# Optimization experiments

Measured on AMD Instinct MI355X. Metric: run time of the kernel, lower is better.

## Reference

```python
import jax, jax.numpy as jnp
import numpy as np

LEAK = 0.01   # torch LeakyReLU default negative_slope
EPS = 1e-5    # torch BatchNorm2d default eps


def setup_inputs() -> dict:
    key = jax.random.key(0)
    ks = jax.random.split(key, 7)
    x = jax.random.normal(ks[0], (1, 64, 512, 512), jnp.float32)
    W = jax.random.normal(ks[1], (128, 64, 3, 3), jnp.float32) * 0.05
    gamma = jax.random.uniform(ks[2], (128,), jnp.float32, 0.5, 1.5)
    beta = jax.random.normal(ks[3], (128,), jnp.float32) * 0.1
    mean = jax.random.normal(ks[4], (128,), jnp.float32) * 0.1
    var = jax.random.uniform(ks[5], (128,), jnp.float32, 0.5, 1.5)
    # random.choices(rate=[0,1,1,...,1]) -> Bernoulli(0.9) mask over (1,C,H*W)
    mask = jax.random.bernoulli(ks[6], 0.9, (1, 128, 512, 512)).astype(jnp.int32)
    return dict(x=x, W=W, gamma=gamma, beta=beta, mean=mean, var=var, mask=mask)


def reference(x, W, gamma, beta, mean, var, mask):
    # 3x3 conv, stride 1, reflect padding 1, no bias
    xp = jnp.pad(x, ((0, 0), (0, 0), (1, 1), (1, 1)), mode='reflect')
    y = jax.lax.conv_general_dilated(
        xp, W, window_strides=(1, 1), padding='VALID',
        dimension_numbers=('NCHW', 'OIHW', 'NCHW'))
    # BatchNorm2d (inference mode: running stats)
    inv = jax.lax.rsqrt(var + EPS)
    scale = (gamma * inv)[None, :, None, None]
    shift = (beta - mean * gamma * inv)[None, :, None, None]
    y = y * scale + shift
    # Dropout2d(0.3) is identity in eval; LeakyReLU
    y = jnp.where(y >= 0, y, LEAK * y)
    # host-generated Bernoulli(0.9) mask multiply (the reshape to (1,C,1,H*W)
    # and back is a no-op on the math)
    return y * mask.astype(y.dtype)
```

## Files before the change

kernel.cpp:

```cpp
#include <hip/hip_runtime.h>

typedef unsigned short u16;
typedef unsigned int u32;
typedef __bf16 bf16x8 __attribute__((ext_vector_type(8)));
typedef float floatx4 __attribute__((ext_vector_type(4)));
typedef int   intx4   __attribute__((ext_vector_type(4)));

#define EPS   1e-5f
#define LEAK  0.01f

#define IN_H   6
#define IN_W   34
#define NPOS   (IN_H * IN_W)
#define CPAD   72
#define CROW   132

#define XT_BYTES ((size_t)512 * 512 * 64 * 2)

__device__ __forceinline__ u16 f2bf(float f) {
    union { float f; u32 i; } v; v.f = f;
    u32 i = v.i;
    return (u16)((i + 0x7fffu + ((i >> 16) & 1u)) >> 16);
}
__device__ __forceinline__ bf16x8 ld_frag(const u16* p) {
    uint4 d = *(const uint4*)p;
    return __builtin_bit_cast(bf16x8, d);
}

__global__ __launch_bounds__(256) void transpose_x(const float* __restrict__ x,
                                                   u16* __restrict__ xt)
{
    __shared__ u32 t[64][65];
    const int tid = threadIdx.x;
    const int s0  = blockIdx.x << 6;

    #pragma unroll
    for (int it = 0; it < 4; ++it) {
        int idx = it * 256 + tid;
        int ci = idx >> 4, wq = idx & 15;
        float4 d = *(const float4*)(x + (ci << 18) + s0 + (wq << 2));
        u32* row = &t[ci][wq << 2];
        row[0] = f2bf(d.x); row[1] = f2bf(d.y);
        row[2] = f2bf(d.z); row[3] = f2bf(d.w);
    }
    __syncthreads();
    #pragma unroll
    for (int it = 0; it < 2; ++it) {
        int idx = it * 256 + tid;
        int sl = idx >> 3, cb = idx & 7;
        uint4 o;
        o.x = t[cb * 8 + 0][sl] | (t[cb * 8 + 1][sl] << 16);
        o.y = t[cb * 8 + 2][sl] | (t[cb * 8 + 3][sl] << 16);
        o.z = t[cb * 8 + 4][sl] | (t[cb * 8 + 5][sl] << 16);
        o.w = t[cb * 8 + 6][sl] | (t[cb * 8 + 7][sl] << 16);
        *(uint4*)(xt + ((s0 + sl) << 6) + (cb << 3)) = o;
    }
}

__global__ __launch_bounds__(256) void transpose_w(const float* __restrict__ w,
                                                   u16* __restrict__ wt)
{
    int idx = blockIdx.x * 256 + threadIdx.x;
    int e   = idx & 7;
    int co  = (idx >> 3) & 127;
    int qk  = idx >> 10;
    int q   = qk & 3;
    int kc  = qk >> 2;
    int r   = kc >> 1;
    int ci  = ((kc & 1) << 5) + (q << 3) + e;
    wt[idx] = f2bf(w[(co << 6 | ci) * 9 + r]);
}

__global__ __launch_bounds__(256, 4) void conv_mfma(
    const u16* __restrict__ xt,   const u16* __restrict__ wt,
    const float* __restrict__ gamma, const float* __restrict__ beta,
    const float* __restrict__ mean,  const float* __restrict__ var,
    const int* __restrict__ mask, float* __restrict__ out)
{
    __shared__ float s_scale[128];
    __shared__ float s_shift[128];
    __shared__ __attribute__((aligned(16))) char smem[64 * CROW * 4];
    u16*   s_tile = (u16*)smem;
    float* cbuf   = (float*)smem;

    const int tid = threadIdx.x;
    const int bid = blockIdx.x;
    const int oh0 = (bid >> 4) << 2;
    const int ow0 = (bid & 15) << 5;

    if (tid < 128) {
        float sc = gamma[tid] * rsqrtf(var[tid] + EPS);
        s_scale[tid] = sc;
        s_shift[tid] = beta[tid] - mean[tid] * sc;
    }

    #pragma unroll
    for (int it = 0; it < 7; ++it) {
        int idx = it * 256 + tid;
        if (idx < NPOS * 8) {
            int pos = idx >> 3, cb = idx & 7;
            int ihl = pos / IN_W;
            int iwl = pos - ihl * IN_W;
            int sh = oh0 - 1 + ihl; sh = sh < 0 ? -sh : (sh > 511 ? 1022 - sh : sh);
            int sw = ow0 - 1 + iwl; sw = sw < 0 ? -sw : (sw > 511 ? 1022 - sw : sw);
            uint4 d = *(const uint4*)(xt + (((sh << 9) + sw) << 6) + (cb << 3));
            *(uint4*)(s_tile + pos * CPAD + (cb << 3)) = d;
        }
    }
    __syncthreads();

    const int wave = tid >> 6;
    const int lane = tid & 63;
    const int quad = lane >> 4;
    const int l16  = lane & 15;
    const int mi   = wave >> 1;
    const int ni   = wave & 1;

    floatx4 acc[4][4];
    #pragma unroll
    for (int i = 0; i < 4; ++i)
        #pragma unroll
        for (int j = 0; j < 4; ++j)
            acc[i][j] = (floatx4){0.f, 0.f, 0.f, 0.f};

    int bbase[4];
    #pragma unroll
    for (int ns = 0; ns < 4; ++ns) {
        int n = ni * 64 + ns * 16 + l16;
        bbase[ns] = ((n >> 5) * IN_W + (n & 31)) * CPAD + quad * 8;
    }
    const u16* abase = wt + (quad << 10) + (mi << 9) + (l16 << 3);

    bf16x8 af_next[4];
    #pragma unroll
    for (int cs = 0; cs < 4; ++cs)
        af_next[cs] = ld_frag(abase + (cs << 7));

    #pragma unroll 1
    for (int kc = 0; kc < 18; ++kc) {
        const int r    = kc >> 1;
        const int kh   = r / 3;
        const int kw   = r - kh * 3;
        const int cib  = (kc & 1) << 5;
        const int boff = (kh * IN_W + kw) * CPAD + cib;

        bf16x8 af[4];
        #pragma unroll
        for (int cs = 0; cs < 4; ++cs) af[cs] = af_next[cs];

        bf16x8 bfr[4];
        #pragma unroll
        for (int ns = 0; ns < 4; ++ns)
            bfr[ns] = ld_frag(s_tile + bbase[ns] + boff);

        if (kc < 17) {
            const int kc1 = kc + 1;
            #pragma unroll
            for (int cs = 0; cs < 4; ++cs)
                af_next[cs] = ld_frag(abase + (kc1 << 12) + (cs << 7));
        }

        #pragma unroll
        for (int cs = 0; cs < 4; ++cs)
            #pragma unroll
            for (int ns = 0; ns < 4; ++ns)
                acc[cs][ns] = __builtin_amdgcn_mfma_f32_16x16x32_bf16(
                    af[cs], bfr[ns], acc[cs][ns], 0, 0, 0);
    }

    __syncthreads();

    #pragma unroll
    for (int c = 0; c < 2; ++c) {
        #pragma unroll
        for (int j = 0; j < 2; ++j) {
            const int cs  = c * 2 + j;
            const int row = mi * 32 + j * 16 + quad * 4;
            #pragma unroll
            for (int ns = 0; ns < 4; ++ns) {
                const int n = ni * 64 + ns * 16 + l16;
                float* p = cbuf + row * CROW + n;
                #pragma unroll
                for (int reg = 0; reg < 4; ++reg)
                    p[reg * CROW] = acc[cs][ns][reg];
            }
        }
        __syncthreads();
        #pragma unroll
        for (int k = 0; k < 8; ++k) {
            const int idx = k * 256 + tid;
            const int row = idx >> 5;
            const int v   = idx & 31;
            floatx4 y4 = *(const floatx4*)(cbuf + row * CROW + (v << 2));
            const int co = ((row >> 5) << 6) + (c << 5) + (row & 31);
            const float sc = s_scale[co], sh = s_shift[co];
            const int gidx = (co << 18) + ((oh0 + (v >> 3)) << 9) + ow0 + ((v & 7) << 2);
            intx4 m = __builtin_nontemporal_load((const intx4*)(mask + gidx));
            floatx4 o;
            float t0 = y4.x * sc + sh; o.x = m.x ? fmaxf(t0, t0 * LEAK) : 0.f;
            float t1 = y4.y * sc + sh; o.y = m.y ? fmaxf(t1, t1 * LEAK) : 0.f;
            float t2 = y4.z * sc + sh; o.z = m.z ? fmaxf(t2, t2 * LEAK) : 0.f;
            float t3 = y4.w * sc + sh; o.w = m.w ? fmaxf(t3, t3 * LEAK) : 0.f;
            __builtin_nontemporal_store(o, (floatx4*)(out + gidx));
        }
        if (c == 0) __syncthreads();
    }
}

extern "C" void kernel_launch(void* const* d_in, const int* in_sizes, int n_in,
                              void* d_out, int out_size, void* d_ws, size_t ws_size,
                              hipStream_t stream)
{
    (void)in_sizes; (void)n_in; (void)out_size; (void)ws_size;
    const float* x     = (const float*)d_in[0];
    const float* W     = (const float*)d_in[1];
    const float* gamma = (const float*)d_in[2];
    const float* beta  = (const float*)d_in[3];
    const float* mean  = (const float*)d_in[4];
    const float* var   = (const float*)d_in[5];
    const int*   mask  = (const int*)d_in[6];
    float* out = (float*)d_out;

    u16* xt = (u16*)d_ws;
    u16* wt = (u16*)((char*)d_ws + XT_BYTES);

    transpose_w<<<288, 256, 0, stream>>>(W, wt);
    transpose_x<<<4096, 256, 0, stream>>>(x, xt);
    conv_mfma<<<2048, 256, 0, stream>>>(xt, wt, gamma, beta, mean, var, mask, out);
}
```

Baseline: 315.6 us.

## Fuse input NCHW-to-bf16 transpose into conv tile load, drop transpose kernel

Removes the separate transpose_x kernel and has each conv block read its fp32 NCHW input halo directly, convert it to bf16 and scatter it into the channel-last shared tile, handling the reflect padding at the borders. This avoids writing and re-reading the 32MB bf16 intermediate and saves one launch. In exchange each block does scalar 2-byte LDS stores with likely bank conflicts, reads roughly 40 columns to cover 34, and repeats the float-to-bf16 conversion for overlapping halos across neighbouring blocks.

```diff
diff --git a/kernel.cpp b/kernel.cpp
--- a/kernel.cpp
+++ b/kernel.cpp
@@ -15,8 +15,6 @@
 #define CPAD   72
 #define CROW   132
 
-#define XT_BYTES ((size_t)512 * 512 * 64 * 2)
-
 __device__ __forceinline__ u16 f2bf(float f) {
     union { float f; u32 i; } v; v.f = f;
     u32 i = v.i;
@@ -25,36 +23,6 @@
 __device__ __forceinline__ bf16x8 ld_frag(const u16* p) {
     uint4 d = *(const uint4*)p;
     return __builtin_bit_cast(bf16x8, d);
-}
-
-__global__ __launch_bounds__(256) void transpose_x(const float* __restrict__ x,
-                                                   u16* __restrict__ xt)
-{
-    __shared__ u32 t[64][65];
-    const int tid = threadIdx.x;
-    const int s0  = blockIdx.x << 6;
-
-    #pragma unroll
-    for (int it = 0; it < 4; ++it) {
-        int idx = it * 256 + tid;
-        int ci = idx >> 4, wq = idx & 15;
-        float4 d = *(const float4*)(x + (ci << 18) + s0 + (wq << 2));
-        u32* row = &t[ci][wq << 2];
-        row[0] = f2bf(d.x); row[1] = f2bf(d.y);
-        row[2] = f2bf(d.z); row[3] = f2bf(d.w);
-    }
-    __syncthreads();
-    #pragma unroll
-    for (int it = 0; it < 2; ++it) {
-        int idx = it * 256 + tid;
-        int sl = idx >> 3, cb = idx & 7;
-        uint4 o;
-        o.x = t[cb * 8 + 0][sl] | (t[cb * 8 + 1][sl] << 16);
-        o.y = t[cb * 8 + 2][sl] | (t[cb * 8 + 3][sl] << 16);
-        o.z = t[cb * 8 + 4][sl] | (t[cb * 8 + 5][sl] << 16);
-        o.w = t[cb * 8 + 6][sl] | (t[cb * 8 + 7][sl] << 16);
-        *(uint4*)(xt + ((s0 + sl) << 6) + (cb << 3)) = o;
-    }
 }
 
 __global__ __launch_bounds__(256) void transpose_w(const float* __restrict__ w,
@@ -72,7 +40,7 @@
 }
 
 __global__ __launch_bounds__(256, 4) void conv_mfma(
-    const u16* __restrict__ xt,   const u16* __restrict__ wt,
+    const float* __restrict__ x,  const u16* __restrict__ wt,
     const float* __restrict__ gamma, const float* __restrict__ beta,
     const float* __restrict__ mean,  const float* __restrict__ var,
     const int* __restrict__ mask, float* __restrict__ out)
@@ -94,17 +62,33 @@
         s_shift[tid] = beta[tid] - mean[tid] * sc;
     }
 
-    #pragma unroll
-    for (int it = 0; it < 7; ++it) {
-        int idx = it * 256 + tid;
-        if (idx < NPOS * 8) {
-            int pos = idx >> 3, cb = idx & 7;
-            int ihl = pos / IN_W;
-            int iwl = pos - ihl * IN_W;
-            int sh = oh0 - 1 + ihl; sh = sh < 0 ? -sh : (sh > 511 ? 1022 - sh : sh);
-            int sw = ow0 - 1 + iwl; sw = sw < 0 ? -sw : (sw > 511 ? 1022 - sw : sw);
-            uint4 d = *(const uint4*)(xt + (((sh << 9) + sw) << 6) + (cb << 3));
-            *(uint4*)(s_tile + pos * CPAD + (cb << 3)) = d;
+    const int wb = (ow0 == 0) ? 0 : ((ow0 == 480) ? 472 : ow0 - 4);
+    #pragma unroll
+    for (int it = 0; it < 3; ++it) {
+        int unit = it * 256 + tid;
+        int row  = unit >> 1;
+        int half = unit & 1;
+        int ci   = row / 6;
+        int ihl  = row - ci * 6;
+        int sh = oh0 - 1 + ihl; sh = sh < 0 ? -sh : (sh > 511 ? 1022 - sh : sh);
+        const int w0 = wb + half * 20;
+        const float* src = x + (ci << 18) + (sh << 9) + w0;
+        #pragma unroll
+        for (int k = 0; k < 5; ++k) {
+            float4 d = *(const float4*)(src + (k << 2));
+            #pragma unroll
+            for (int j = 0; j < 4; ++j) {
+                float f = (j == 0) ? d.x : (j == 1) ? d.y : (j == 2) ? d.z : d.w;
+                const int w  = w0 + (k << 2) + j;
+                const int wl = w - ow0 + 1;
+                const u16 b = f2bf(f);
+                if (wl >= 0 && wl < IN_W)
+                    s_tile[(ihl * IN_W + wl) * CPAD + ci] = b;
+                if (ow0 == 0 && w == 1)
+                    s_tile[(ihl * IN_W + 0) * CPAD + ci] = b;
+                if (ow0 == 480 && w == 510)
+                    s_tile[(ihl * IN_W + 33) * CPAD + ci] = b;
+            }
         }
     }
     __syncthreads();
@@ -221,10 +205,8 @@
     const int*   mask  = (const int*)d_in[6];
     float* out = (float*)d_out;
 
-    u16* xt = (u16*)d_ws;
-    u16* wt = (u16*)((char*)d_ws + XT_BYTES);
+    u16* wt = (u16*)d_ws;
 
     transpose_w<<<288, 256, 0, stream>>>(W, wt);
-    transpose_x<<<4096, 256, 0, stream>>>(x, xt);
-    conv_mfma<<<2048, 256, 0, stream>>>(xt, wt, gamma, beta, mean, var, mask, out);
-}
+    conv_mfma<<<2048, 256, 0, stream>>>(x, wt, gamma, beta, mean, var, mask, out);
+}
```

After: 323.1 us. 2.4% more time.
